# Kernel optimization log

Measured on AMD Instinct MI355X. Metric: run time of the kernel, lower is better.

The kernel has to match this reference:

```python
import jax, jax.numpy as jnp
import numpy as np

N, S, R, K, D = 1024, 144, 96, 128, 768
COMPONENT_PADDING = 0.0


def setup_inputs() -> dict:
    rng = np.random.default_rng(0)
    residual_indices = np.sort(rng.choice(S, R, replace=False)).astype(np.int64)
    ablated_indices = np.setdiff1d(np.arange(S, dtype=np.int64), residual_indices)
    basis_lengths = (64 + (np.arange(R) % 65)).astype(np.int32)  # ragged, in [64,128]
    total = int(basis_lengths.sum())

    key = jax.random.key(0)
    kx, kb, km, kl = jax.random.split(key, 4)
    x = jax.random.normal(kx, (N, S, D), dtype=jnp.float32)
    bases = jax.random.normal(kb, (R, K, D), dtype=jnp.float32) / np.sqrt(D).astype(np.float32)
    # K != D branch: pseudo-inverse-style projection back  (R,K,D)
    gram = jnp.einsum('rkd,rjd->rkj', bases, bases)  # (R,K,K)
    inv_bases = jnp.einsum('rkj,rjd->rkd', jnp.linalg.inv(gram), bases)
    means = 0.02 * jax.random.normal(km, (R, D), dtype=jnp.float32)
    lambdas = jax.random.normal(kl, (total,), dtype=jnp.float32) + 1.0

    return {
        'x': x,
        'lambdas': lambdas,
        'bases': bases,
        'inv_bases': inv_bases,
        'means': means,
        'residual_indices': jnp.asarray(residual_indices),
        'ablated_indices': jnp.asarray(ablated_indices),
        'basis_lengths': jnp.asarray(basis_lengths),
    }


def _padded_lambdas(lambdas, basis_lengths, k):
    # emulate split + pad_sequence + F.pad: (R, K) with padding_value on tail
    lengths = basis_lengths.astype(jnp.int32)
    offsets = jnp.concatenate([jnp.zeros((1,), jnp.int32), jnp.cumsum(lengths)[:-1]])
    pos = jnp.arange(k, dtype=jnp.int32)            # (K,)
    valid = pos[None, :] < lengths[:, None]          # (R,K)
    idx = jnp.clip(offsets[:, None] + pos[None, :], 0, lambdas.shape[0] - 1)
    return jnp.where(valid, lambdas[idx], jnp.float32(COMPONENT_PADDING))


def reference(x, lambdas, bases, inv_bases, means, residual_indices, ablated_indices, basis_lengths):
    r, k, d = bases.shape
    unit_lambdas = _padded_lambdas(lambdas, basis_lengths, k)       # (R,K)
    adapted = x[:, residual_indices, :] - means[None]                # (N,R,D)
    coeffs = jnp.einsum('nrd,rkd->nrk', adapted, bases * unit_lambdas[:, :, None])
    recon = jnp.einsum('nrk,rkd->nrd', coeffs, inv_bases)            # (N,R,D)
    out = recon.sum(axis=1)                                          # (N,D)
    out = out + x[:, ablated_indices, :].sum(axis=1)                 # ablation=None -> add complement sum
    return out
```

## Files before the change

kernel.cpp:

```cpp
#include <hip/hip_runtime.h>

static constexpr int N_ = 1024;
static constexpr int S_ = 144;
static constexpr int R_ = 96;
static constexpr int K_ = 128;
static constexpr int D_ = 768;

typedef __attribute__((ext_vector_type(8))) short short8;
typedef __attribute__((ext_vector_type(4))) short short4_t;
typedef __attribute__((ext_vector_type(4))) float floatx4;

__device__ inline short f2bf(float f) {
  unsigned u = __builtin_bit_cast(unsigned, f);
  return (short)((u + 0x7FFFu + ((u >> 16) & 1u)) >> 16);
}

__global__ __launch_bounds__(256) void k_pad_lambdas(
    const float* __restrict__ lambdas, const int* __restrict__ lens,
    float* __restrict__ ul) {
  __shared__ int offs[R_];
  if (threadIdx.x == 0) {
    int acc = 0;
    for (int r = 0; r < R_; ++r) { offs[r] = acc; acc += lens[r]; }
  }
  __syncthreads();
  for (int i = threadIdx.x; i < R_ * K_; i += 256) {
    int r = i >> 7;
    int k = i & (K_ - 1);
    float v = 0.0f;
    if (k < lens[r]) v = lambdas[offs[r] + k];
    ul[i] = v;
  }
}

__global__ __launch_bounds__(256) void k_cvt_bases(
    const float* __restrict__ bases, const float* __restrict__ ul,
    short* __restrict__ bbf) {
  size_t i = ((size_t)blockIdx.x * 256 + threadIdx.x) * 4;
  if (i >= (size_t)R_ * K_ * D_) return;
  int rk = (int)(i / D_);
  float s = ul[rk];
  float4 v = *(const float4*)(bases + i);
  short4_t o;
  o.x = f2bf(v.x * s); o.y = f2bf(v.y * s);
  o.z = f2bf(v.z * s); o.w = f2bf(v.w * s);
  *(short4_t*)(bbf + i) = o;
}

__global__ __launch_bounds__(256) void k_trans_inv(
    const float* __restrict__ invb, short* __restrict__ ibt) {
  const int d0 = blockIdx.x * 32;
  const int k0 = blockIdx.y * 32;
  const int r  = blockIdx.z;
  __shared__ short tile[32][33];
  const int t = threadIdx.x;
  {
    int kr = t >> 3;
    int dg = (t & 7) * 4;
    float4 v = *(const float4*)(invb + ((size_t)r * K_ + k0 + kr) * D_ + d0 + dg);
    tile[kr][dg + 0] = f2bf(v.x);
    tile[kr][dg + 1] = f2bf(v.y);
    tile[kr][dg + 2] = f2bf(v.z);
    tile[kr][dg + 3] = f2bf(v.w);
  }
  __syncthreads();
  {
    int dr = t >> 3;
    int kg = (t & 7) * 4;
    short4_t o;
    o.x = tile[kg + 0][dr]; o.y = tile[kg + 1][dr];
    o.z = tile[kg + 2][dr]; o.w = tile[kg + 3][dr];
    *(short4_t*)(ibt + (size_t)(d0 + dr) * (R_ * K_) + r * K_ + k0 + kg) = o;
  }
}

__global__ __launch_bounds__(256) void k_ablated(
    const float* __restrict__ x, const int* __restrict__ abl,
    float* __restrict__ out, int nab) {
  int i = blockIdx.x * 256 + threadIdx.x;
  const int nd4 = N_ * D_ / 4;
  if (i >= nd4) return;
  int n = i / (D_ / 4);
  int d4 = i - n * (D_ / 4);
  const float4* xr = (const float4*)x;
  size_t base = (size_t)n * (S_ * D_ / 4) + d4;
  float4 acc = make_float4(0.f, 0.f, 0.f, 0.f);
  for (int j = 0; j < nab; ++j) {
    float4 v = xr[base + (size_t)abl[j] * (D_ / 4)];
    acc.x += v.x; acc.y += v.y; acc.z += v.z; acc.w += v.w;
  }
  ((float4*)out)[i] = acc;
}

__global__ __launch_bounds__(256) void k1_mfma(
    const float* __restrict__ x, const short* __restrict__ bbf,
    const float* __restrict__ means, const int* __restrict__ resi,
    short* __restrict__ coeffs) {
  const int r  = blockIdx.y;
  const int n0 = blockIdx.x * 128;
  const int s  = resi[r];

  __shared__ short As[128][72];
  __shared__ short Bs[128][72];

  const int t = threadIdx.x;
  const int wid = t >> 6, l = t & 63;
  const int wr = wid >> 1, wc = wid & 1;
  const int lm = l & 15, quad = l >> 4;

  floatx4 acc[4][4];
#pragma unroll
  for (int i = 0; i < 4; ++i)
#pragma unroll
    for (int j = 0; j < 4; ++j) acc[i][j] = (floatx4)(0.0f);

  const int arow = t >> 4;
  const int acol = (t & 15) * 4;
  const int brow = t >> 3;
  const int bcol = (t & 7) * 8;

  const float* xb = x + (size_t)s * D_;
  const short* bb = bbf + (size_t)r * K_ * D_;
  const float* mb = means + (size_t)r * D_;

  for (int d0 = 0; d0 < D_; d0 += 64) {
    float4 mv = *(const float4*)(mb + d0 + acol);
#pragma unroll
    for (int rr = 0; rr < 8; ++rr) {
      int row = arow + rr * 16;
      float4 xv = *(const float4*)(xb + (size_t)(n0 + row) * (S_ * D_) + d0 + acol);
      short4_t v;
      v.x = f2bf(xv.x - mv.x); v.y = f2bf(xv.y - mv.y);
      v.z = f2bf(xv.z - mv.z); v.w = f2bf(xv.w - mv.w);
      *(short4_t*)&As[row][acol] = v;
    }
#pragma unroll
    for (int rr = 0; rr < 4; ++rr) {
      int row = brow + rr * 32;
      short8 v = *(const short8*)(bb + (size_t)row * D_ + d0 + bcol);
      *(short8*)&Bs[row][bcol] = v;
    }
    __syncthreads();
#pragma unroll
    for (int kk = 0; kk < 2; ++kk) {
      short8 af[4], bf[4];
#pragma unroll
      for (int i = 0; i < 4; ++i)
        af[i] = *(const short8*)&As[wr * 64 + i * 16 + lm][kk * 32 + quad * 8];
#pragma unroll
      for (int j = 0; j < 4; ++j)
        bf[j] = *(const short8*)&Bs[wc * 64 + j * 16 + lm][kk * 32 + quad * 8];
#pragma unroll
      for (int i = 0; i < 4; ++i)
#pragma unroll
        for (int j = 0; j < 4; ++j)
          acc[i][j] = __builtin_amdgcn_mfma_f32_16x16x32_bf16(
              af[i], bf[j], acc[i][j], 0, 0, 0);
    }
    __syncthreads();
  }

#pragma unroll
  for (int i = 0; i < 4; ++i) {
    int row = n0 + wr * 64 + i * 16 + quad * 4;
#pragma unroll
    for (int j = 0; j < 4; ++j) {
      int col = r * K_ + wc * 64 + j * 16 + lm;
#pragma unroll
      for (int g = 0; g < 4; ++g)
        coeffs[(size_t)(row + g) * (R_ * K_) + col] = f2bf(acc[i][j][g]);
    }
  }
}

static constexpr int SPLITK = 8;
static constexpr int KC = R_ * K_ / SPLITK;

__global__ __launch_bounds__(256) void k2_mfma(
    const short* __restrict__ coeffs, const short* __restrict__ ibt,
    float* __restrict__ out) {
  const int n0  = blockIdx.x * 128;
  const int dd0 = blockIdx.y * 128;
  const int kc0 = blockIdx.z * KC;
  const int ldk = R_ * K_;

  __shared__ short As[128][72];
  __shared__ short Bs[128][72];

  const int t = threadIdx.x;
  const int wid = t >> 6, l = t & 63;
  const int wr = wid >> 1, wc = wid & 1;
  const int lm = l & 15, quad = l >> 4;

  floatx4 acc[4][4];
#pragma unroll
  for (int i = 0; i < 4; ++i)
#pragma unroll
    for (int j = 0; j < 4; ++j) acc[i][j] = (floatx4)(0.0f);

  const int srow = t >> 3;
  const int scol = (t & 7) * 8;

  for (int k0 = kc0; k0 < kc0 + KC; k0 += 64) {
#pragma unroll
    for (int rr = 0; rr < 4; ++rr) {
      int row = srow + rr * 32;
      short8 a = *(const short8*)(coeffs + (size_t)(n0 + row) * ldk + k0 + scol);
      *(short8*)&As[row][scol] = a;
      short8 b = *(const short8*)(ibt + (size_t)(dd0 + row) * ldk + k0 + scol);
      *(short8*)&Bs[row][scol] = b;
    }
    __syncthreads();
#pragma unroll
    for (int kk = 0; kk < 2; ++kk) {
      short8 af[4], bf[4];
#pragma unroll
      for (int i = 0; i < 4; ++i)
        af[i] = *(const short8*)&As[wr * 64 + i * 16 + lm][kk * 32 + quad * 8];
#pragma unroll
      for (int j = 0; j < 4; ++j)
        bf[j] = *(const short8*)&Bs[wc * 64 + j * 16 + lm][kk * 32 + quad * 8];
#pragma unroll
      for (int i = 0; i < 4; ++i)
#pragma unroll
        for (int j = 0; j < 4; ++j)
          acc[i][j] = __builtin_amdgcn_mfma_f32_16x16x32_bf16(
              af[i], bf[j], acc[i][j], 0, 0, 0);
    }
    __syncthreads();
  }

#pragma unroll
  for (int i = 0; i < 4; ++i) {
    int row = n0 + wr * 64 + i * 16 + quad * 4;
#pragma unroll
    for (int j = 0; j < 4; ++j) {
      int col = dd0 + wc * 64 + j * 16 + lm;
#pragma unroll
      for (int g = 0; g < 4; ++g)
        atomicAdd(&out[(size_t)(row + g) * D_ + col], acc[i][j][g]);
    }
  }
}

__global__ __launch_bounds__(256) void k_pass1(
    const float* __restrict__ x, const float* __restrict__ bases,
    const float* __restrict__ means, const int* __restrict__ resi,
    const float* __restrict__ ul, float* __restrict__ coeffs,
    int r0, int Rc) {
  const int rz = blockIdx.z;
  const int r  = r0 + rz;
  const int n0 = blockIdx.x * 64;
  const int k0 = blockIdx.y * 64;
  const int s  = resi[r];
  __shared__ float As[64][33];
  __shared__ float Bs[64][33];
  const int t  = threadIdx.x;
  const int tx = t & 15, ty = t >> 4;
  const int lc = (t & 7) * 4;
  const int lr = t >> 3;
  const float* xbase = x + (size_t)s * D_;
  const float* bbase = bases + ((size_t)r * K_ + k0) * D_;
  const float* mbase = means + (size_t)r * D_;
  float acc[4][4] = {};
  for (int d0 = 0; d0 < D_; d0 += 32) {
    float4 mv = *(const float4*)(mbase + d0 + lc);
#pragma unroll
    for (int rr = 0; rr < 2; ++rr) {
      int row = lr + rr * 32;
      float4 xv = *(const float4*)(xbase + (size_t)(n0 + row) * (S_ * D_) + d0 + lc);
      As[row][lc + 0] = xv.x - mv.x; As[row][lc + 1] = xv.y - mv.y;
      As[row][lc + 2] = xv.z - mv.z; As[row][lc + 3] = xv.w - mv.w;
      float4 bv = *(const float4*)(bbase + (size_t)row * D_ + d0 + lc);
      Bs[row][lc + 0] = bv.x; Bs[row][lc + 1] = bv.y;
      Bs[row][lc + 2] = bv.z; Bs[row][lc + 3] = bv.w;
    }
    __syncthreads();
#pragma unroll
    for (int dd = 0; dd < 32; ++dd) {
      float a[4], b[4];
#pragma unroll
      for (int i = 0; i < 4; ++i) a[i] = As[ty * 4 + i][dd];
#pragma unroll
      for (int j = 0; j < 4; ++j) b[j] = Bs[tx * 4 + j][dd];
#pragma unroll
      for (int i = 0; i < 4; ++i)
#pragma unroll
        for (int j = 0; j < 4; ++j) acc[i][j] = fmaf(a[i], b[j], acc[i][j]);
    }
    __syncthreads();
  }
  const int ldc = Rc * K_;
#pragma unroll
  for (int i = 0; i < 4; ++i) {
    int n = n0 + ty * 4 + i;
#pragma unroll
    for (int j = 0; j < 4; ++j) {
      int k = k0 + tx * 4 + j;
      coeffs[(size_t)n * ldc + rz * K_ + k] = ul[r * K_ + k] * acc[i][j];
    }
  }
}

__global__ __launch_bounds__(256) void k_pass2(
    const float* __restrict__ coeffs, const float* __restrict__ invb,
    float* __restrict__ out, int Kg) {
  const int n0 = blockIdx.x * 64;
  const int d0 = blockIdx.y * 64;
  __shared__ float As[64][33];
  __shared__ float Bs[32][65];
  const int t  = threadIdx.x;
  const int tx = t & 15, ty = t >> 4;
  const int lca = (t & 7) * 4;
  const int lra = t >> 3;
  const int lcb = (t & 15) * 4;
  const int lrb = t >> 4;
  float acc[4][4] = {};
  for (int kk0 = 0; kk0 < Kg; kk0 += 32) {
#pragma unroll
    for (int rr = 0; rr < 2; ++rr) {
      int row = lra + rr * 32;
      float4 av = *(const float4*)(coeffs + (size_t)(n0 + row) * Kg + kk0 + lca);
      As[row][lca + 0] = av.x; As[row][lca + 1] = av.y;
      As[row][lca + 2] = av.z; As[row][lca + 3] = av.w;
      int brow = lrb + rr * 16;
      float4 bv = *(const float4*)(invb + (size_t)(kk0 + brow) * D_ + d0 + lcb);
      Bs[brow][lcb + 0] = bv.x; Bs[brow][lcb + 1] = bv.y;
      Bs[brow][lcb + 2] = bv.z; Bs[brow][lcb + 3] = bv.w;
    }
    __syncthreads();
#pragma unroll
    for (int kk = 0; kk < 32; ++kk) {
      float a[4], b[4];
#pragma unroll
      for (int i = 0; i < 4; ++i) a[i] = As[ty * 4 + i][kk];
#pragma unroll
      for (int j = 0; j < 4; ++j) b[j] = Bs[kk][tx * 4 + j];
#pragma unroll
      for (int i = 0; i < 4; ++i)
#pragma unroll
        for (int j = 0; j < 4; ++j) acc[i][j] = fmaf(a[i], b[j], acc[i][j]);
    }
    __syncthreads();
  }
#pragma unroll
  for (int i = 0; i < 4; ++i) {
    int n = n0 + ty * 4 + i;
#pragma unroll
    for (int j = 0; j < 4; ++j) {
      int d = d0 + tx * 4 + j;
      out[(size_t)n * D_ + d] += acc[i][j];
    }
  }
}

__global__ __launch_bounds__(256) void k_fused(
    const float* __restrict__ x, const float* __restrict__ bases,
    const float* __restrict__ invb, const float* __restrict__ means,
    const int* __restrict__ resi, const float* __restrict__ lambdas,
    const int* __restrict__ lens, float* __restrict__ out) {
  const int r  = blockIdx.y;
  const int n0 = blockIdx.x * 64;
  const int s  = resi[r];
  __shared__ float As[64][33];
  __shared__ float Bs[128][33];
  __shared__ float Cs[64][132];
  __shared__ float lam[K_];
  __shared__ int offS;
  const int t  = threadIdx.x;
  if (t == 0) {
    int o = 0;
    for (int i = 0; i < r; ++i) o += lens[i];
    offS = o;
  }
  __syncthreads();
  if (t < K_) lam[t] = (t < lens[r]) ? lambdas[offS + t] : 0.0f;
  const int lc = (t & 7) * 4;
  const int lr = t >> 3;
  const float* mbase = means + (size_t)r * D_;
  const float* bbase = bases + (size_t)r * K_ * D_;
  const int tx = t & 15, ty = t >> 4;
  float acc[4][8] = {};
  for (int d0 = 0; d0 < D_; d0 += 32) {
    float4 mv = *(const float4*)(mbase + d0 + lc);
#pragma unroll
    for (int rr = 0; rr < 2; ++rr) {
      int row = lr + rr * 32;
      float4 xv = *(const float4*)(x + ((size_t)(n0 + row) * S_ + s) * D_ + d0 + lc);
      As[row][lc + 0] = xv.x - mv.x; As[row][lc + 1] = xv.y - mv.y;
      As[row][lc + 2] = xv.z - mv.z; As[row][lc + 3] = xv.w - mv.w;
    }
#pragma unroll
    for (int rr = 0; rr < 4; ++rr) {
      int row = lr + rr * 32;
      float4 bv = *(const float4*)(bbase + (size_t)row * D_ + d0 + lc);
      Bs[row][lc + 0] = bv.x; Bs[row][lc + 1] = bv.y;
      Bs[row][lc + 2] = bv.z; Bs[row][lc + 3] = bv.w;
    }
    __syncthreads();
#pragma unroll
    for (int dd = 0; dd < 32; ++dd) {
      float a[4], b[8];
#pragma unroll
      for (int i = 0; i < 4; ++i) a[i] = As[ty * 4 + i][dd];
#pragma unroll
      for (int j = 0; j < 8; ++j) b[j] = Bs[tx * 8 + j][dd];
#pragma unroll
      for (int i = 0; i < 4; ++i)
#pragma unroll
        for (int j = 0; j < 8; ++j) acc[i][j] = fmaf(a[i], b[j], acc[i][j]);
    }
    __syncthreads();
  }
#pragma unroll
  for (int i = 0; i < 4; ++i)
#pragma unroll
    for (int j = 0; j < 8; ++j)
      Cs[ty * 4 + i][tx * 8 + j] = lam[tx * 8 + j] * acc[i][j];
  __syncthreads();
  const float* ibase = invb + (size_t)r * K_ * D_;
  const int tx2 = t & 15;
  for (int d0 = 0; d0 < D_; d0 += 32) {
#pragma unroll
    for (int rr = 0; rr < 4; ++rr) {
      int row = lr + rr * 32;
      float4 bv = *(const float4*)(ibase + (size_t)row * D_ + d0 + lc);
      Bs[row][lc + 0] = bv.x; Bs[row][lc + 1] = bv.y;
      Bs[row][lc + 2] = bv.z; Bs[row][lc + 3] = bv.w;
    }
    __syncthreads();
    float c[4][2] = {};
#pragma unroll
    for (int k = 0; k < K_; ++k) {
      float a[4], b[2];
#pragma unroll
      for (int i = 0; i < 4; ++i) a[i] = Cs[ty * 4 + i][k];
#pragma unroll
      for (int j = 0; j < 2; ++j) b[j] = Bs[k][tx2 * 2 + j];
#pragma unroll
      for (int i = 0; i < 4; ++i)
#pragma unroll
        for (int j = 0; j < 2; ++j) c[i][j] = fmaf(a[i], b[j], c[i][j]);
    }
#pragma unroll
    for (int i = 0; i < 4; ++i)
#pragma unroll
      for (int j = 0; j < 2; ++j)
        atomicAdd(&out[(size_t)(n0 + ty * 4 + i) * D_ + d0 + tx2 * 2 + j], c[i][j]);
    __syncthreads();
  }
}

extern "C" void kernel_launch(void* const* d_in, const int* in_sizes, int n_in,
                              void* d_out, int out_size, void* d_ws, size_t ws_size,
                              hipStream_t stream) {
  const float* x       = (const float*)d_in[0];
  const float* lambdas = (const float*)d_in[1];
  const float* bases   = (const float*)d_in[2];
  const float* invb    = (const float*)d_in[3];
  const float* means   = (const float*)d_in[4];
  const int*   resi    = (const int*)d_in[5];
  const int*   abl     = (const int*)d_in[6];
  const int*   lens    = (const int*)d_in[7];
  float* out = (float*)d_out;
  const int nab = in_sizes[6];

  const size_t ul_b  = (size_t)R_ * K_ * sizeof(float);
  const size_t bbf_b = (size_t)R_ * K_ * D_ * sizeof(short);
  const size_t ibt_b = (size_t)D_ * R_ * K_ * sizeof(short);
  const size_t cf_b  = (size_t)N_ * R_ * K_ * sizeof(short);
  const size_t need  = ul_b + bbf_b + ibt_b + cf_b;

  k_ablated<<<(N_ * D_ / 4 + 255) / 256, 256, 0, stream>>>(x, abl, out, nab);

  if (ws_size >= need) {
    float* ul   = (float*)d_ws;
    short* bbf  = (short*)((char*)d_ws + ul_b);
    short* ibt  = (short*)((char*)d_ws + ul_b + bbf_b);
    short* cfs  = (short*)((char*)d_ws + ul_b + bbf_b + ibt_b);

    k_pad_lambdas<<<1, 256, 0, stream>>>(lambdas, lens, ul);
    k_cvt_bases<<<(R_ * K_ * D_ / 4 + 255) / 256, 256, 0, stream>>>(bases, ul, bbf);
    dim3 gt(D_ / 32, K_ / 32, R_);
    k_trans_inv<<<gt, 256, 0, stream>>>(invb, ibt);
    dim3 g1(N_ / 128, R_);
    k1_mfma<<<g1, 256, 0, stream>>>(x, bbf, means, resi, cfs);
    dim3 g2(N_ / 128, D_ / 128, SPLITK);
    k2_mfma<<<g2, 256, 0, stream>>>(cfs, ibt, out);
    return;
  }

  const size_t per_r = (size_t)N_ * K_ * sizeof(float);
  if (ws_size >= ul_b + per_r) {
    float* ul = (float*)d_ws;
    float* coeffs = (float*)((char*)d_ws + ul_b);
    int Rc = (int)((ws_size - ul_b) / per_r);
    if (Rc > R_) Rc = R_;
    k_pad_lambdas<<<1, 256, 0, stream>>>(lambdas, lens, ul);
    for (int r0 = 0; r0 < R_; r0 += Rc) {
      int rc = (R_ - r0 < Rc) ? (R_ - r0) : Rc;
      dim3 g1(N_ / 64, K_ / 64, rc);
      k_pass1<<<g1, 256, 0, stream>>>(x, bases, means, resi, ul, coeffs, r0, rc);
      dim3 g2(N_ / 64, D_ / 64);
      k_pass2<<<g2, 256, 0, stream>>>(coeffs, invb + (size_t)r0 * K_ * D_, out,
                                      rc * K_);
    }
  } else {
    dim3 g(N_ / 64, R_);
    k_fused<<<g, 256, 0, stream>>>(x, bases, invb, means, resi, lambdas, lens,
                                   out);
  }
}
```

Measured before the change: 747.9 us.

## Stage GEMM tiles with direct global-to-LDS loads and vectorize coeff stores

Replaces the register round-trip tile staging in both MFMA GEMM kernels with global_load_lds direct-to-LDS copies, using unpadded 64-wide shared tiles, and falls back to plain copies if the builtin is missing. In k1 it also swaps the MFMA operand order so each lane holds four consecutive k values, which allows packed short4 stores of coeffs instead of scalar strided stores. Dropping the padding may bring back LDS bank conflicts on the fragment reads, and the 16-byte direct-to-LDS width depends on hardware and compiler support.

```diff
diff --git a/kernel.cpp b/kernel.cpp
--- a/kernel.cpp
+++ b/kernel.cpp
@@ -13,6 +13,25 @@
 __device__ inline short f2bf(float f) {
   unsigned u = __builtin_bit_cast(unsigned, f);
   return (short)((u + 0x7FFFu + ((u >> 16) & 1u)) >> 16);
+}
+
+#if defined(__has_builtin)
+#if __has_builtin(__builtin_amdgcn_global_load_lds)
+#define HAS_GLL 1
+#endif
+#endif
+#ifndef HAS_GLL
+#define HAS_GLL 0
+#endif
+
+__device__ __forceinline__ void stage16(const void* g, void* lds_base, int lane) {
+#if HAS_GLL
+  __builtin_amdgcn_global_load_lds(
+      (const __attribute__((address_space(1))) void*)g,
+      (__attribute__((address_space(3))) void*)lds_base, 16, 0, 0);
+#else
+  *(short8*)((short*)lds_base + lane * 8) = *(const short8*)g;
+#endif
 }
 
 __global__ __launch_bounds__(256) void k_pad_lambdas(
@@ -99,9 +118,10 @@
   const int r  = blockIdx.y;
   const int n0 = blockIdx.x * 128;
   const int s  = resi[r];
+  const int ldk = R_ * K_;
 
   __shared__ short As[128][72];
-  __shared__ short Bs[128][72];
+  __shared__ short Bs[128][64];
 
   const int t = threadIdx.x;
   const int wid = t >> 6, l = t & 63;
@@ -116,14 +136,20 @@
 
   const int arow = t >> 4;
   const int acol = (t & 15) * 4;
-  const int brow = t >> 3;
-  const int bcol = (t & 7) * 8;
 
   const float* xb = x + (size_t)s * D_;
   const short* bb = bbf + (size_t)r * K_ * D_;
   const float* mb = means + (size_t)r * D_;
 
+  const int srow = l >> 3;
+  const int scol = (l & 7) * 8;
+
   for (int d0 = 0; d0 < D_; d0 += 64) {
+#pragma unroll
+    for (int ii = 0; ii < 4; ++ii) {
+      int rb = wid * 32 + ii * 8;
+      stage16(bb + (size_t)(rb + srow) * D_ + d0 + scol, &Bs[rb][0], l);
+    }
     float4 mv = *(const float4*)(mb + d0 + acol);
 #pragma unroll
     for (int rr = 0; rr < 8; ++rr) {
@@ -134,12 +160,6 @@
       v.z = f2bf(xv.z - mv.z); v.w = f2bf(xv.w - mv.w);
       *(short4_t*)&As[row][acol] = v;
     }
-#pragma unroll
-    for (int rr = 0; rr < 4; ++rr) {
-      int row = brow + rr * 32;
-      short8 v = *(const short8*)(bb + (size_t)row * D_ + d0 + bcol);
-      *(short8*)&Bs[row][bcol] = v;
-    }
     __syncthreads();
 #pragma unroll
     for (int kk = 0; kk < 2; ++kk) {
@@ -155,20 +175,21 @@
 #pragma unroll
         for (int j = 0; j < 4; ++j)
           acc[i][j] = __builtin_amdgcn_mfma_f32_16x16x32_bf16(
-              af[i], bf[j], acc[i][j], 0, 0, 0);
+              bf[j], af[i], acc[i][j], 0, 0, 0);
     }
     __syncthreads();
   }
 
 #pragma unroll
   for (int i = 0; i < 4; ++i) {
-    int row = n0 + wr * 64 + i * 16 + quad * 4;
+    int n = n0 + wr * 64 + i * 16 + lm;
 #pragma unroll
     for (int j = 0; j < 4; ++j) {
-      int col = r * K_ + wc * 64 + j * 16 + lm;
-#pragma unroll
-      for (int g = 0; g < 4; ++g)
-        coeffs[(size_t)(row + g) * (R_ * K_) + col] = f2bf(acc[i][j][g]);
+      int kb = wc * 64 + j * 16 + quad * 4;
+      short4_t v;
+      v.x = f2bf(acc[i][j][0]); v.y = f2bf(acc[i][j][1]);
+      v.z = f2bf(acc[i][j][2]); v.w = f2bf(acc[i][j][3]);
+      *(short4_t*)&coeffs[(size_t)n * ldk + r * K_ + kb] = v;
     }
   }
 }
@@ -184,8 +205,8 @@
   const int kc0 = blockIdx.z * KC;
   const int ldk = R_ * K_;
 
-  __shared__ short As[128][72];
-  __shared__ short Bs[128][72];
+  __shared__ short As[128][64];
+  __shared__ short Bs[128][64];
 
   const int t = threadIdx.x;
   const int wid = t >> 6, l = t & 63;
@@ -198,17 +219,15 @@
 #pragma unroll
     for (int j = 0; j < 4; ++j) acc[i][j] = (floatx4)(0.0f);
 
-  const int srow = t >> 3;
-  const int scol = (t & 7) * 8;
+  const int srow = l >> 3;
+  const int scol = (l & 7) * 8;
 
   for (int k0 = kc0; k0 < kc0 + KC; k0 += 64) {
 #pragma unroll
-    for (int rr = 0; rr < 4; ++rr) {
-      int row = srow + rr * 32;
-      short8 a = *(const short8*)(coeffs + (size_t)(n0 + row) * ldk + k0 + scol);
-      *(short8*)&As[row][scol] = a;
-      short8 b = *(const short8*)(ibt + (size_t)(dd0 + row) * ldk + k0 + scol);
-      *(short8*)&Bs[row][scol] = b;
+    for (int ii = 0; ii < 4; ++ii) {
+      int rb = wid * 32 + ii * 8;
+      stage16(coeffs + (size_t)(n0 + rb + srow) * ldk + k0 + scol, &As[rb][0], l);
+      stage16(ibt + (size_t)(dd0 + rb + srow) * ldk + k0 + scol, &Bs[rb][0], l);
     }
     __syncthreads();
 #pragma unroll
```

After: 755.4 us. No clear change (+1.0%).
